# Performance work log

Hardware: AMD Instinct MI355X
Metric: run time of the kernel (lower is better)

The kernel has to match this reference:

```python
import jax, jax.numpy as jnp
import numpy as np

B, S, H = 16, 1024, 64
HEADS, DH = 4, 16
EPS = 1e-5


def _layernorm(x, g, b):
    mu = jnp.mean(x, axis=-1, keepdims=True)
    var = jnp.mean(jnp.square(x - mu), axis=-1, keepdims=True)
    return (x - mu) * jax.lax.rsqrt(var + EPS) * g + b


def setup_inputs() -> dict:
    key = jax.random.key(0)
    ks = jax.random.split(key, 16)
    s = 1.0 / np.sqrt(H)
    inp = {
        'x': jax.random.normal(ks[0], (B, S, H), dtype=jnp.float32),
        'lengths': jax.random.randint(ks[1], (B,), 1, S + 1, dtype=jnp.int32),
        'atten': jnp.zeros((1,), dtype=jnp.float32),  # unused placeholder arg
        'Wq': jax.random.normal(ks[2], (H, H), dtype=jnp.float32) * s,
        'bq': jnp.zeros((H,), dtype=jnp.float32),
        'Wk': jax.random.normal(ks[3], (H, H), dtype=jnp.float32) * s,
        'bk': jnp.zeros((H,), dtype=jnp.float32),
        'Wv': jax.random.normal(ks[4], (H, H), dtype=jnp.float32) * s,
        'bv': jnp.zeros((H,), dtype=jnp.float32),
        'W1': jax.random.normal(ks[5], (H, H), dtype=jnp.float32) * s,
        'b1': jnp.zeros((H,), dtype=jnp.float32),
        'W2': jax.random.normal(ks[6], (H, H), dtype=jnp.float32) * s,
        'b2': jnp.zeros((H,), dtype=jnp.float32),
        'g1': jnp.ones((H,), dtype=jnp.float32),
        'be1': jnp.zeros((H,), dtype=jnp.float32),
        'g2': jnp.ones((H,), dtype=jnp.float32),
        'be2': jnp.zeros((H,), dtype=jnp.float32),
    }
    return inp


def reference(x, lengths, atten, Wq, bq, Wk, bk, Wv, bv, W1, b1, W2, b2, g1, be1, g2, be2):
    del atten  # overwritten in original forward before any use
    b, s, h = x.shape

    def proj(W, bias):
        p = x @ W.T + bias  # [b,s,h]
        return p.reshape(b, s, HEADS, DH).transpose(0, 2, 1, 3)  # [b,nh,s,dh]

    q, k, v = proj(Wq, bq), proj(Wk, bk), proj(Wv, bv)
    scores = jnp.einsum('bhqd,bhkd->bhqk', q, k) / np.float32(np.sqrt(h))

    causal = jnp.tril(jnp.ones((s, s), dtype=bool))  # [s,s]
    pos = jnp.arange(s)
    valid = pos[None, :] < lengths[:, None]  # [b,s]
    mask = causal[None, None] & valid[:, None, None, :] & valid[:, None, :, None]

    logits = jnp.where(mask, scores, jnp.float32(-1e30))
    att = jax.nn.softmax(logits, axis=-1) * mask  # zero fully-masked rows (NaN->0 trick)

    out = jnp.einsum('bhqk,bhkd->bhqd', att, v)
    out = out.transpose(0, 2, 1, 3).reshape(b, s, h)

    out_1 = x + out  # dropout is identity in eval mode
    out_1_norm = _layernorm(out_1, g1, be1)
    ff = jax.nn.gelu(out_1_norm @ W1.T + b1, approximate=False) @ W2.T + b2
    y_prim = _layernorm(out_1_norm + ff, g2, be2)

    atten_mean = jnp.mean(att, axis=1)  # [b,s,s], detached in original
    return (y_prim, atten_mean)
```

## Files before the change

### kernel.cpp

```cpp
#include <hip/hip_runtime.h>

#define NB 16
#define NS 1024
#define NHID 64
#define NHEADS 4
#define NDH 16
#define LN_EPS 1e-5f
#define QSCALE 0.18033688011112f

using v2h  = __attribute__((ext_vector_type(2))) _Float16;
using v4h  = __attribute__((ext_vector_type(4))) _Float16;
using v4f  = __attribute__((ext_vector_type(4))) float;

__device__ __forceinline__ v4h cvt4h(float4 a) {
    v4h r; r[0] = (_Float16)a.x; r[1] = (_Float16)a.y;
    r[2] = (_Float16)a.z; r[3] = (_Float16)a.w; return r;
}

__global__ __launch_bounds__(256) void qkv_mfma_kernel(
    const float* __restrict__ x,
    const float* __restrict__ Wq, const float* __restrict__ bq,
    const float* __restrict__ Wk, const float* __restrict__ bk,
    const float* __restrict__ Wv, const float* __restrict__ bv,
    _Float16* __restrict__ qh, _Float16* __restrict__ kh,
    _Float16* __restrict__ vt)
{
    const int t = threadIdx.x;
    const int w = t >> 6, l = t & 63;
    const int n16 = l & 15, g = l >> 4;
    const int rt = (int)blockIdx.x * 4 + w;
    const int srow0 = rt * 16;
    const int b = srow0 >> 10, s0 = srow0 & 1023;
    const size_t sg = (size_t)srow0 + n16;

    v4h xa[4];
    #pragma unroll
    for (int kb = 0; kb < 4; ++kb)
        xa[kb] = cvt4h(*(const float4*)&x[sg * 64 + kb * 16 + 4 * g]);

    #pragma unroll
    for (int m = 0; m < 3; ++m) {
        const float* W  = (m == 0) ? Wq : (m == 1) ? Wk : Wv;
        const float* bb = (m == 0) ? bq : (m == 1) ? bk : bv;
        #pragma unroll
        for (int mb = 0; mb < 4; ++mb) {
            const float4 bv4 = *(const float4*)&bb[mb * 16 + 4 * g];
            v4f acc = {bv4.x, bv4.y, bv4.z, bv4.w};
            #pragma unroll
            for (int kb = 0; kb < 4; ++kb) {
                v4h wf = cvt4h(*(const float4*)&W[(size_t)(mb * 16 + n16) * 64 + kb * 16 + 4 * g]);
                acc = __builtin_amdgcn_mfma_f32_16x16x16f16(wf, xa[kb], acc, 0, 0, 0);
            }
            const size_t hb = (size_t)(b * NHEADS + mb);
            if (m == 0) {
                v4h r = {(_Float16)(acc[0] * QSCALE), (_Float16)(acc[1] * QSCALE),
                         (_Float16)(acc[2] * QSCALE), (_Float16)(acc[3] * QSCALE)};
                *(v4h*)&qh[(hb * NS + s0 + n16) * NDH + 4 * g] = r;
            } else if (m == 1) {
                v4h r = {(_Float16)acc[0], (_Float16)acc[1], (_Float16)acc[2], (_Float16)acc[3]};
                *(v4h*)&kh[(hb * NS + s0 + n16) * NDH + 4 * g] = r;
            } else {
                #pragma unroll
                for (int i = 0; i < 4; ++i)
                    vt[(hb * NDH + 4 * g + i) * NS + s0 + n16] = (_Float16)acc[i];
            }
        }
    }
}

__global__ __launch_bounds__(1024, 8) void attn_ffn_kernel(
    const _Float16* __restrict__ qh, const _Float16* __restrict__ kh,
    const _Float16* __restrict__ vt, const int* __restrict__ lengths,
    const float* __restrict__ x,
    const float* __restrict__ W1, const float* __restrict__ b1,
    const float* __restrict__ W2, const float* __restrict__ b2,
    const float* __restrict__ g1, const float* __restrict__ be1,
    const float* __restrict__ g2, const float* __restrict__ be2,
    float* __restrict__ amean,
    float* __restrict__ y)
{
    __shared__ __align__(16) _Float16 Plds[2][NHEADS][16][72];
    __shared__ float zlds[4][NHEADS][16];
    __shared__ float aout_s[16][68];
    __shared__ __align__(16) _Float16 h1s[4][16][20];
    __shared__ float ln2s[4][16][2];

    const int t = threadIdx.x;
    const int wv = t >> 6;
    const int h  = wv & 3;
    const int kq = wv >> 2;
    const int l  = t & 63;
    const int g = l >> 4, n16 = l & 15;
    const int qt = 63 - (int)blockIdx.x;
    const int b  = blockIdx.y;
    const int len = lengths[b];
    const int q0 = qt << 4;
    const int qA_ = q0 + n16;
    const bool qvA = qA_ < len;
    const bool lenFA = len >= q0 + 16;

    const size_t hbase = ((size_t)(b * NHEADS + h)) * NS;
    const v4h QA = *(const v4h*)&qh[(hbase + qA_) * NDH + 4 * g];

    const int nkA = (len <= q0) ? 0 : min(q0 + 16, len);
    const int ntA = (nkA + 63) >> 6;
    const v4f z4v = {0.f, 0.f, 0.f, 0.f};

    float ZA = 0.f;
    for (int tile = 0; tile < ntA; ++tile) {
        const int ks = (tile << 6) + (kq << 4);
        if (ks >= nkA) continue;
        const v4h K = *(const v4h*)&kh[(hbase + ks + n16) * NDH + 4 * g];
        v4f st = __builtin_amdgcn_mfma_f32_16x16x16f16(K, QA, z4v, 0, 0, 0);
        if (lenFA && (ks + 15 <= q0)) {
            ZA += exp2f(st[0]) + exp2f(st[1]) + exp2f(st[2]) + exp2f(st[3]);
        } else {
            #pragma unroll
            for (int i = 0; i < 4; ++i) {
                int kg = ks + 4 * g + i;
                ZA += (qvA && kg <= qA_) ? exp2f(st[i]) : 0.f;
            }
        }
    }
    ZA += __shfl_xor(ZA, 16, 64); ZA += __shfl_xor(ZA, 32, 64);
    if (l < 16) zlds[kq][h][n16] = ZA;
    __syncthreads();
    const float ztA = zlds[0][h][n16] + zlds[1][h][n16]
                    + zlds[2][h][n16] + zlds[3][h][n16];
    const float izA = (ztA > 0.f) ? 1.f / ztA : 0.f;

    v4f oA = z4v;
    const int pc = (kq << 4) + 4 * g;
    for (int tile = 0; tile < ntA; ++tile) {
        const int k0 = tile << 6;
        const int ks = k0 + (kq << 4);
        const int par = tile & 1;
        v4h phA = {(_Float16)0.f, (_Float16)0.f, (_Float16)0.f, (_Float16)0.f};
        if (ks < nkA) {
            const v4h K = *(const v4h*)&kh[(hbase + ks + n16) * NDH + 4 * g];
            const v4h V = *(const v4h*)&vt[(((size_t)(b * NHEADS + h)) * NDH + n16) * NS + ks + 4 * g];
            v4f st = __builtin_amdgcn_mfma_f32_16x16x16f16(K, QA, z4v, 0, 0, 0);
            float p0, p1, p2, p3;
            if (lenFA && (ks + 15 <= q0)) {
                p0 = exp2f(st[0]) * izA; p1 = exp2f(st[1]) * izA;
                p2 = exp2f(st[2]) * izA; p3 = exp2f(st[3]) * izA;
            } else {
                const int kg = ks + 4 * g;
                p0 = (qvA && kg + 0 <= qA_) ? exp2f(st[0]) * izA : 0.f;
                p1 = (qvA && kg + 1 <= qA_) ? exp2f(st[1]) * izA : 0.f;
                p2 = (qvA && kg + 2 <= qA_) ? exp2f(st[2]) * izA : 0.f;
                p3 = (qvA && kg + 3 <= qA_) ? exp2f(st[3]) * izA : 0.f;
            }
            phA[0] = (_Float16)p0; phA[1] = (_Float16)p1;
            phA[2] = (_Float16)p2; phA[3] = (_Float16)p3;
            oA = __builtin_amdgcn_mfma_f32_16x16x16f16(phA, V, oA, 0, 0, 0);
        }
        *(v4h*)&Plds[par][h][n16][pc] = phA;
        __syncthreads();
        {
            const int r = t >> 6, c = t & 63;
            float s = (float)Plds[par][0][r][c] + (float)Plds[par][1][r][c]
                    + (float)Plds[par][2][r][c] + (float)Plds[par][3][r][c];
            amean[((size_t)(b * NS + q0 + r)) * NS + k0 + c] = 0.25f * s;
        }
    }
    __syncthreads();

    float* obuf = (float*)Plds;
    {
        float* p = &obuf[(wv * 64 + l) * 4];
        p[0] = oA[0]; p[1] = oA[1]; p[2] = oA[2]; p[3] = oA[3];
    }
    __syncthreads();
    if (kq == 0) {
        #pragma unroll
        for (int kq2 = 1; kq2 < 4; ++kq2) {
            const float* p = &obuf[(((h + 4 * kq2) * 64) + l) * 4];
            oA[0] += p[0]; oA[1] += p[1]; oA[2] += p[2]; oA[3] += p[3];
        }
        #pragma unroll
        for (int i = 0; i < 4; ++i)
            aout_s[4 * g + i][h * 16 + n16] = oA[i];
    }
    __syncthreads();

    const bool fact = wv < 4;
    const int fw = wv;
    const size_t row = (size_t)(b * NS + q0) + n16;

    v4h n1h[4];
    float4 n1self;
    if (fact) {
        float4 o1f[4];
        #pragma unroll
        for (int kb = 0; kb < 4; ++kb) {
            float4 xv = *(const float4*)&x[row * 64 + kb * 16 + 4 * g];
            float4 av = *(const float4*)&aout_s[n16][kb * 16 + 4 * g];
            o1f[kb] = make_float4(xv.x + av.x, xv.y + av.y, xv.z + av.z, xv.w + av.w);
        }
        float s = 0.f;
        #pragma unroll
        for (int kb = 0; kb < 4; ++kb) s += o1f[kb].x + o1f[kb].y + o1f[kb].z + o1f[kb].w;
        s += __shfl_xor(s, 16, 64); s += __shfl_xor(s, 32, 64);
        const float mu = s * (1.f / 64.f);
        float vs = 0.f;
        #pragma unroll
        for (int kb = 0; kb < 4; ++kb) {
            float a = o1f[kb].x - mu, bb = o1f[kb].y - mu, c = o1f[kb].z - mu, d = o1f[kb].w - mu;
            vs += a * a + bb * bb + c * c + d * d;
        }
        vs += __shfl_xor(vs, 16, 64); vs += __shfl_xor(vs, 32, 64);
        const float rs = rsqrtf(vs * (1.f / 64.f) + LN_EPS);
        #pragma unroll
        for (int kb = 0; kb < 4; ++kb) {
            float4 gv  = *(const float4*)&g1[kb * 16 + 4 * g];
            float4 bev = *(const float4*)&be1[kb * 16 + 4 * g];
            float4 nv;
            nv.x = (o1f[kb].x - mu) * rs * gv.x + bev.x;
            nv.y = (o1f[kb].y - mu) * rs * gv.y + bev.y;
            nv.z = (o1f[kb].z - mu) * rs * gv.z + bev.z;
            nv.w = (o1f[kb].w - mu) * rs * gv.w + bev.w;
            n1h[kb] = cvt4h(nv);
            if (kb == fw) n1self = nv;
        }
        const float4 b1v = *(const float4*)&b1[fw * 16 + 4 * g];
        v4f acc = {b1v.x, b1v.y, b1v.z, b1v.w};
        #pragma unroll
        for (int kb = 0; kb < 4; ++kb) {
            v4h wf = cvt4h(*(const float4*)&W1[(size_t)(fw * 16 + n16) * 64 + kb * 16 + 4 * g]);
            acc = __builtin_amdgcn_mfma_f32_16x16x16f16(wf, n1h[kb], acc, 0, 0, 0);
        }
        v4h hh;
        #pragma unroll
        for (int i = 0; i < 4; ++i) {
            float a = acc[i];
            hh[i] = (_Float16)(0.5f * a * (1.f + erff(a * 0.70710678118654752f)));
        }
        *(v4h*)&h1s[fw][n16][4 * g] = hh;
    } else {
        const int kz = ntA << 6;
        const int nz4 = (NS - kz) >> 2;
        const float4 zf = make_float4(0.f, 0.f, 0.f, 0.f);
        const int tt = (wv - 4) * 64 + l;
        for (int r = 0; r < 16; ++r)
            for (int c4 = tt; c4 < nz4; c4 += 768)
                *(float4*)&amean[((size_t)(b * NS + q0 + r)) * NS + kz + c4 * 4] = zf;
    }
    __syncthreads();

    float4 zrow;
    if (fact) {
        const float4 b2v = *(const float4*)&b2[fw * 16 + 4 * g];
        v4f acc = {b2v.x, b2v.y, b2v.z, b2v.w};
        #pragma unroll
        for (int db = 0; db < 4; ++db) {
            v4h hf = *(const v4h*)&h1s[db][n16][4 * g];
            v4h wf = cvt4h(*(const float4*)&W2[(size_t)(fw * 16 + n16) * 64 + db * 16 + 4 * g]);
            acc = __builtin_amdgcn_mfma_f32_16x16x16f16(wf, hf, acc, 0, 0, 0);
        }
        zrow = make_float4(n1self.x + acc[0], n1self.y + acc[1],
                           n1self.z + acc[2], n1self.w + acc[3]);
        float s2 = zrow.x + zrow.y + zrow.z + zrow.w;
        float q2 = zrow.x * zrow.x + zrow.y * zrow.y + zrow.z * zrow.z + zrow.w * zrow.w;
        s2 += __shfl_xor(s2, 16, 64); s2 += __shfl_xor(s2, 32, 64);
        q2 += __shfl_xor(q2, 16, 64); q2 += __shfl_xor(q2, 32, 64);
        if (g == 0) { ln2s[fw][n16][0] = s2; ln2s[fw][n16][1] = q2; }
    }
    __syncthreads();
    if (fact) {
        const float ts = ln2s[0][n16][0] + ln2s[1][n16][0]
                       + ln2s[2][n16][0] + ln2s[3][n16][0];
        const float tq = ln2s[0][n16][1] + ln2s[1][n16][1]
                       + ln2s[2][n16][1] + ln2s[3][n16][1];
        const float mu2 = ts * (1.f / 64.f);
        const float var2 = tq * (1.f / 64.f) - mu2 * mu2;
        const float rs2 = rsqrtf(var2 + LN_EPS);
        float4 gv  = *(const float4*)&g2[fw * 16 + 4 * g];
        float4 bev = *(const float4*)&be2[fw * 16 + 4 * g];
        float4 yv;
        yv.x = (zrow.x - mu2) * rs2 * gv.x + bev.x;
        yv.y = (zrow.y - mu2) * rs2 * gv.y + bev.y;
        yv.z = (zrow.z - mu2) * rs2 * gv.z + bev.z;
        yv.w = (zrow.w - mu2) * rs2 * gv.w + bev.w;
        *(float4*)&y[row * 64 + fw * 16 + 4 * g] = yv;
    }
}

extern "C" void kernel_launch(void* const* d_in, const int* in_sizes, int n_in,
                              void* d_out, int out_size, void* d_ws, size_t ws_size,
                              hipStream_t stream) {
    const float* x   = (const float*)d_in[0];
    const int* lengths = (const int*)d_in[1];
    const float* Wq  = (const float*)d_in[3];
    const float* bq  = (const float*)d_in[4];
    const float* Wk  = (const float*)d_in[5];
    const float* bk  = (const float*)d_in[6];
    const float* Wv  = (const float*)d_in[7];
    const float* bv  = (const float*)d_in[8];
    const float* W1  = (const float*)d_in[9];
    const float* b1  = (const float*)d_in[10];
    const float* W2  = (const float*)d_in[11];
    const float* b2  = (const float*)d_in[12];
    const float* g1  = (const float*)d_in[13];
    const float* be1 = (const float*)d_in[14];
    const float* g2  = (const float*)d_in[15];
    const float* be2 = (const float*)d_in[16];

    float* y     = (float*)d_out;
    float* amean = y + (size_t)NB * NS * NHID;

    const size_t nqkv = (size_t)NB * NHEADS * NS * NDH;
    _Float16* qhw = (_Float16*)d_ws;
    _Float16* khw = qhw + nqkv;
    _Float16* vtw = khw + nqkv;

    hipLaunchKernelGGL(qkv_mfma_kernel, dim3(NB * NS / 64), dim3(256), 0, stream,
                       x, Wq, bq, Wk, bk, Wv, bv, qhw, khw, vtw);
    hipLaunchKernelGGL(attn_ffn_kernel, dim3(64, NB), dim3(1024), 0, stream,
                       qhw, khw, vtw, lengths, x,
                       W1, b1, W2, b2, g1, be1, g2, be2,
                       amean, y);
}
```

Baseline: 60.90 us.

## Fuse softmax normalizer pass into single QK/PV pass with deferred normalization

Drops the separate pass that computed the softmax denominator. Now one pass computes unnormalized exp scores, accumulates both the denominator and P·V, and keeps the fp16 probabilities in registers (16 tiles). Normalization is applied afterwards: the attention output is scaled by 1/Z per head, and the amean writes scale each head's stored P by its own 1/Z. amean now runs on a 4-buffer LDS ring with a barrier every two tiles instead of every tile. This removes the recomputation of QK and exp and halves the block barriers, at the cost of more registers (which may lower occupancy at 1024 threads) and unnormalized fp16 exp values that could lose precision or overflow. Because no row max is subtracted, the fp16 range risk was already present before.

```diff
diff --git a/kernel.cpp b/kernel.cpp
--- a/kernel.cpp
+++ b/kernel.cpp
@@ -8,7 +8,6 @@
 #define LN_EPS 1e-5f
 #define QSCALE 0.18033688011112f
 
-using v2h  = __attribute__((ext_vector_type(2))) _Float16;
 using v4h  = __attribute__((ext_vector_type(4))) _Float16;
 using v4f  = __attribute__((ext_vector_type(4))) float;
 
@@ -79,13 +78,14 @@
     float* __restrict__ amean,
     float* __restrict__ y)
 {
-    __shared__ __align__(16) _Float16 Plds[2][NHEADS][16][72];
+    __shared__ __align__(16) _Float16 Plds[4][NHEADS][16][72];
     __shared__ float zlds[4][NHEADS][16];
+    __shared__ float iz_s[NHEADS][16];
     __shared__ float aout_s[16][68];
     __shared__ __align__(16) _Float16 h1s[4][16][20];
     __shared__ float ln2s[4][16][2];
 
-    const int t = threadIdx.x;
+    const int t  = threadIdx.x;
     const int wv = t >> 6;
     const int h  = wv & 3;
     const int kq = wv >> 2;
@@ -98,70 +98,76 @@
     const int qA_ = q0 + n16;
     const bool qvA = qA_ < len;
     const bool lenFA = len >= q0 + 16;
-
-    const size_t hbase = ((size_t)(b * NHEADS + h)) * NS;
-    const v4h QA = *(const v4h*)&qh[(hbase + qA_) * NDH + 4 * g];
-
     const int nkA = (len <= q0) ? 0 : min(q0 + 16, len);
     const int ntA = (nkA + 63) >> 6;
+
+    const size_t hbase = ((size_t)(b * NHEADS + h)) * NS;
+    const size_t vbase = ((size_t)(b * NHEADS + h)) * NDH + n16;
+    const v4h QA = *(const v4h*)&qh[(hbase + qA_) * NDH + 4 * g];
     const v4f z4v = {0.f, 0.f, 0.f, 0.f};
+    const int pc = (kq << 4) + 4 * g;
 
     float ZA = 0.f;
-    for (int tile = 0; tile < ntA; ++tile) {
+    v4f oA = z4v;
+    v4h preg[16];
+    #pragma unroll
+    for (int tile = 0; tile < 16; ++tile) {
+        v4h ph = {(_Float16)0.f, (_Float16)0.f, (_Float16)0.f, (_Float16)0.f};
         const int ks = (tile << 6) + (kq << 4);
-        if (ks >= nkA) continue;
-        const v4h K = *(const v4h*)&kh[(hbase + ks + n16) * NDH + 4 * g];
-        v4f st = __builtin_amdgcn_mfma_f32_16x16x16f16(K, QA, z4v, 0, 0, 0);
-        if (lenFA && (ks + 15 <= q0)) {
-            ZA += exp2f(st[0]) + exp2f(st[1]) + exp2f(st[2]) + exp2f(st[3]);
-        } else {
-            #pragma unroll
-            for (int i = 0; i < 4; ++i) {
-                int kg = ks + 4 * g + i;
-                ZA += (qvA && kg <= qA_) ? exp2f(st[i]) : 0.f;
-            }
-        }
-    }
-    ZA += __shfl_xor(ZA, 16, 64); ZA += __shfl_xor(ZA, 32, 64);
-    if (l < 16) zlds[kq][h][n16] = ZA;
-    __syncthreads();
-    const float ztA = zlds[0][h][n16] + zlds[1][h][n16]
-                    + zlds[2][h][n16] + zlds[3][h][n16];
-    const float izA = (ztA > 0.f) ? 1.f / ztA : 0.f;
-
-    v4f oA = z4v;
-    const int pc = (kq << 4) + 4 * g;
-    for (int tile = 0; tile < ntA; ++tile) {
-        const int k0 = tile << 6;
-        const int ks = k0 + (kq << 4);
-        const int par = tile & 1;
-        v4h phA = {(_Float16)0.f, (_Float16)0.f, (_Float16)0.f, (_Float16)0.f};
-        if (ks < nkA) {
+        if (tile < ntA && ks < nkA) {
             const v4h K = *(const v4h*)&kh[(hbase + ks + n16) * NDH + 4 * g];
-            const v4h V = *(const v4h*)&vt[(((size_t)(b * NHEADS + h)) * NDH + n16) * NS + ks + 4 * g];
+            const v4h V = *(const v4h*)&vt[vbase * NS + ks + 4 * g];
             v4f st = __builtin_amdgcn_mfma_f32_16x16x16f16(K, QA, z4v, 0, 0, 0);
             float p0, p1, p2, p3;
             if (lenFA && (ks + 15 <= q0)) {
-                p0 = exp2f(st[0]) * izA; p1 = exp2f(st[1]) * izA;
-                p2 = exp2f(st[2]) * izA; p3 = exp2f(st[3]) * izA;
+                p0 = exp2f(st[0]); p1 = exp2f(st[1]);
+                p2 = exp2f(st[2]); p3 = exp2f(st[3]);
             } else {
                 const int kg = ks + 4 * g;
-                p0 = (qvA && kg + 0 <= qA_) ? exp2f(st[0]) * izA : 0.f;
-                p1 = (qvA && kg + 1 <= qA_) ? exp2f(st[1]) * izA : 0.f;
-                p2 = (qvA && kg + 2 <= qA_) ? exp2f(st[2]) * izA : 0.f;
-                p3 = (qvA && kg + 3 <= qA_) ? exp2f(st[3]) * izA : 0.f;
+                p0 = (qvA && kg + 0 <= qA_) ? exp2f(st[0]) : 0.f;
+                p1 = (qvA && kg + 1 <= qA_) ? exp2f(st[1]) : 0.f;
+                p2 = (qvA && kg + 2 <= qA_) ? exp2f(st[2]) : 0.f;
+                p3 = (qvA && kg + 3 <= qA_) ? exp2f(st[3]) : 0.f;
             }
-            phA[0] = (_Float16)p0; phA[1] = (_Float16)p1;
-            phA[2] = (_Float16)p2; phA[3] = (_Float16)p3;
-            oA = __builtin_amdgcn_mfma_f32_16x16x16f16(phA, V, oA, 0, 0, 0);
-        }
-        *(v4h*)&Plds[par][h][n16][pc] = phA;
-        __syncthreads();
-        {
+            ZA += p0 + p1 + p2 + p3;
+            ph[0] = (_Float16)p0; ph[1] = (_Float16)p1;
+            ph[2] = (_Float16)p2; ph[3] = (_Float16)p3;
+            oA = __builtin_amdgcn_mfma_f32_16x16x16f16(ph, V, oA, 0, 0, 0);
+        }
+        preg[tile] = ph;
+    }
+    ZA += __shfl_xor(ZA, 16, 64); ZA += __shfl_xor(ZA, 32, 64);
+    if (l < 16) zlds[kq][h][l] = ZA;
+    __syncthreads();
+    if (t < 64) {
+        const int hh = t >> 4, qq = t & 15;
+        const float z = zlds[0][hh][qq] + zlds[1][hh][qq]
+                      + zlds[2][hh][qq] + zlds[3][hh][qq];
+        iz_s[hh][qq] = (z > 0.f) ? 1.f / z : 0.f;
+    }
+
+    #pragma unroll
+    for (int tile = 0; tile < 16; ++tile) {
+        const int buf = tile & 3;
+        if (tile < ntA)
+            *(v4h*)&Plds[buf][h][n16][pc] = preg[tile];
+        if ((tile & 1) == 1 && (tile - 1) < ntA) {
+            __syncthreads();
             const int r = t >> 6, c = t & 63;
-            float s = (float)Plds[par][0][r][c] + (float)Plds[par][1][r][c]
-                    + (float)Plds[par][2][r][c] + (float)Plds[par][3][r][c];
-            amean[((size_t)(b * NS + q0 + r)) * NS + k0 + c] = 0.25f * s;
+            const float i0 = iz_s[0][r], i1 = iz_s[1][r],
+                        i2 = iz_s[2][r], i3 = iz_s[3][r];
+            #pragma unroll
+            for (int it = 0; it < 2; ++it) {
+                const int tf = tile - 1 + it;
+                if (tf < ntA) {
+                    const int bf = tf & 3;
+                    float s = (float)Plds[bf][0][r][c] * i0
+                            + (float)Plds[bf][1][r][c] * i1
+                            + (float)Plds[bf][2][r][c] * i2
+                            + (float)Plds[bf][3][r][c] * i3;
+                    amean[((size_t)(b * NS + q0 + r)) * NS + (tf << 6) + c] = 0.25f * s;
+                }
+            }
         }
     }
     __syncthreads();
@@ -180,7 +186,7 @@
         }
         #pragma unroll
         for (int i = 0; i < 4; ++i)
-            aout_s[4 * g + i][h * 16 + n16] = oA[i];
+            aout_s[4 * g + i][h * 16 + n16] = oA[i] * iz_s[h][4 * g + i];
     }
     __syncthreads();
 
```

Result: faster. 51.91 us (median of 2 runs) (-14.8%).
